# Kernel tuning notes

Hardware: AMD Instinct MI355X
Metric: run time of the kernel (lower is better)

## Reference

```python
import jax, jax.numpy as jnp
import numpy as np

N_NODES = 100000
N_EDGES = 300000
D_IN = 256
D_OUT = 256
NEG_SLOPE = 0.2


def setup_inputs() -> dict:
    key = jax.random.key(0)
    ks = jax.random.split(key, 6)
    feat = jax.random.normal(ks[0], (N_NODES, D_IN), dtype=jnp.float32)
    # xavier-normal-ish init scale
    scale = (2.0 / (D_IN + D_OUT)) ** 0.5
    W_src = jax.random.normal(ks[1], (D_IN, D_OUT), dtype=jnp.float32) * scale
    b_src = jnp.zeros((D_OUT,), dtype=jnp.float32)
    W_dst = jax.random.normal(ks[2], (D_IN, D_OUT), dtype=jnp.float32) * scale
    b_dst = jnp.zeros((D_OUT,), dtype=jnp.float32)
    attn = jax.random.normal(ks[3], (D_OUT,), dtype=jnp.float32) * scale
    src = jax.random.randint(ks[4], (N_EDGES,), 0, N_NODES, dtype=jnp.int32)
    dst = jax.random.randint(ks[5], (N_EDGES,), 0, N_NODES, dtype=jnp.int32)
    return {"feat": feat, "W_src": W_src, "b_src": b_src,
            "W_dst": W_dst, "b_dst": b_dst, "attn": attn,
            "src": src, "dst": dst}


def reference(feat, W_src, b_src, W_dst, b_dst, attn, src, dst):
    N = feat.shape[0]
    # node projections (dense GEMMs)
    el = feat @ W_src + b_src          # [N, D_OUT]  (feat_src / 'el')
    er = feat @ W_dst + b_dst          # [N, D_OUT]  (feat_dst / 'er')
    # edge-wise u_add_v + LeakyReLU, then attention dot
    e = jax.nn.leaky_relu(el[src] + er[dst], NEG_SLOPE)  # [E, D_OUT]
    score = e @ attn                    # [E]  ((e*attn).sum(-1))
    # edge softmax segmented by destination node
    smax = jax.ops.segment_max(score, dst, num_segments=N)   # [N]
    ex = jnp.exp(score - smax[dst])                           # [E]
    ssum = jax.ops.segment_sum(ex, dst, num_segments=N)      # [N]
    a = ex / ssum[dst]                                        # [E]
    # weighted scatter-sum aggregation: u_mul_e('el','a') -> sum per dst
    out = jax.ops.segment_sum(el[src] * a[:, None], dst, num_segments=N)
    return out  # [N, D_OUT]
```

## Files before the change

### kernel.cpp

```cpp
#include <hip/hip_runtime.h>
#include <cstdint>
#include <cmath>

#define D 256
#define NEG 0.2f
#define BK 64
#define NT (D/BK)

typedef __attribute__((ext_vector_type(8))) __bf16 bf16x8;
typedef __attribute__((ext_vector_type(8))) unsigned short ushort8;
typedef __attribute__((ext_vector_type(4))) float f32x4;

__device__ __forceinline__ unsigned short f2bf(float f){
    unsigned u = __float_as_uint(f);
    return (unsigned short)((u + 0x7fffu + ((u >> 16) & 1u)) >> 16);
}
__device__ __forceinline__ float b2f(unsigned short u){
    return __uint_as_float(((unsigned)u) << 16);
}

__device__ __forceinline__ void gload_lds16(const void* g, void* l){
    __builtin_amdgcn_global_load_lds(
        (const __attribute__((address_space(1))) unsigned int*)g,
        (__attribute__((address_space(3))) unsigned int*)l, 16, 0, 0);
}

__global__ __launch_bounds__(256) void prep_all_kernel(
    const float* __restrict__ Wsrc, const float* __restrict__ Wdst,
    const float* __restrict__ bsrc, const float* __restrict__ bdst,
    unsigned short* __restrict__ WT, float* __restrict__ biascat,
    const float* __restrict__ feat, unsigned short* __restrict__ featb,
    int N, int NPAD,
    const int* __restrict__ dst, int* __restrict__ deg, int E, int CB)
{
    const int b = blockIdx.x;
    if (b < 64) {
        int idx = b*256 + threadIdx.x;
        int col = idx >> 5;
        int u   = idx & 31;
        int gu  = (u & 24) | ((u ^ col) & 7);
        const float* W = (col < 256) ? Wsrc : Wdst;
        int c = col & 255;
        ushort8 o;
        #pragma unroll
        for (int j = 0; j < 8; ++j)
            o[j] = f2bf(W[(size_t)(gu*8 + j)*D + c]);
        *(ushort8*)(WT + (size_t)col*D + u*8) = o;
        if (idx < 512) biascat[idx] = (idx < 256) ? bsrc[idx] : bdst[idx-256];
    } else if (b < 64 + CB) {
        int e = (b - 64)*256 + threadIdx.x;
        if (e < E) atomicAdd(&deg[dst[e]], 1);
    } else {
        int nfb   = gridDim.x - 64 - CB;
        int total = NPAD * 32;
        for (int idx = (b - 64 - CB)*256 + threadIdx.x; idx < total; idx += nfb*256){
            int r = idx >> 5;
            int u = idx & 31;
            ushort8 o;
            if (r < N){
                int gu = (u & 24) | ((u ^ r) & 7);
                const float* s = feat + (size_t)r*D + gu*8;
                float4 a = *(const float4*)s;
                float4 bb = *(const float4*)(s + 4);
                o[0]=f2bf(a.x); o[1]=f2bf(a.y); o[2]=f2bf(a.z); o[3]=f2bf(a.w);
                o[4]=f2bf(bb.x); o[5]=f2bf(bb.y); o[6]=f2bf(bb.z); o[7]=f2bf(bb.w);
            } else {
                #pragma unroll
                for (int j = 0; j < 8; ++j) o[j] = 0;
            }
            *(ushort8*)(featb + (size_t)r*D + u*8) = o;
        }
    }
}

__global__ __launch_bounds__(256) void proj_mfma_kernel(
    const unsigned short* __restrict__ featb, const unsigned short* __restrict__ WT,
    const float* __restrict__ biascat,
    unsigned short* __restrict__ el16, unsigned short* __restrict__ er16, int N)
{
    __shared__ unsigned short As[2][128*BK];
    __shared__ unsigned short Bs[2][128*BK];

    const int b    = blockIdx.x;
    const int xcd  = b & 7;
    const int s    = b >> 3;
    const int p    = (s >> 2)*8 + xcd;
    const int c    = s & 3;
    const int row0 = p * 128;
    const int col0 = c * 128;

    const int tid  = threadIdx.x;
    const int wave = tid >> 6;
    const int lane = tid & 63;
    const int wr = (wave >> 1) * 64;
    const int wc = (wave & 1) * 64;
    const int l15 = lane & 15;
    const int kg  = lane >> 4;

    const int sr = (wave << 3) + (lane >> 3);
    const int sc = (lane & 7) * 8;

    f32x4 acc[4][4] = {};

    #pragma unroll
    for (int r4 = 0; r4 < 4; ++r4) {
        int ar = r4*32 + sr;
        gload_lds16(featb + (size_t)(row0 + ar)*D + 0 + sc, &As[0][(r4*32 + wave*8)*BK]);
        gload_lds16(WT    + (size_t)(col0 + ar)*D + 0 + sc, &Bs[0][(r4*32 + wave*8)*BK]);
    }

    for (int t = 0; t < NT; ++t) {
        const int cur = t & 1;
        if (t + 1 < NT) {
            int k0 = (t + 1) * BK;
            #pragma unroll
            for (int r4 = 0; r4 < 4; ++r4) {
                int ar = r4*32 + sr;
                gload_lds16(featb + (size_t)(row0 + ar)*D + k0 + sc,
                            &As[cur ^ 1][(r4*32 + wave*8)*BK]);
                gload_lds16(WT    + (size_t)(col0 + ar)*D + k0 + sc,
                            &Bs[cur ^ 1][(r4*32 + wave*8)*BK]);
            }
            asm volatile("s_waitcnt vmcnt(8)" ::: "memory");
        } else {
            asm volatile("s_waitcnt vmcnt(0)" ::: "memory");
        }
        __builtin_amdgcn_s_barrier();
        __builtin_amdgcn_sched_barrier(0);

        #pragma unroll
        for (int ks = 0; ks < 2; ++ks) {
            bf16x8 af[4], bfr[4];
            #pragma unroll
            for (int m = 0; m < 4; ++m){
                int row = wr + m*16 + l15;
                int cc = ((kg + ks*4) ^ (row & 7)) * 8;
                af[m] = *(const bf16x8*)&As[cur][row*BK + cc];
            }
            #pragma unroll
            for (int n = 0; n < 4; ++n){
                int row = wc + n*16 + l15;
                int cc = ((kg + ks*4) ^ (row & 7)) * 8;
                bfr[n] = *(const bf16x8*)&Bs[cur][row*BK + cc];
            }
            #pragma unroll
            for (int m = 0; m < 4; ++m)
                #pragma unroll
                for (int n = 0; n < 4; ++n)
                    acc[m][n] = __builtin_amdgcn_mfma_f32_16x16x32_bf16(bfr[n], af[m], acc[m][n], 0, 0, 0);
        }
        __builtin_amdgcn_sched_barrier(0);
        __builtin_amdgcn_s_barrier();
    }

    unsigned short* __restrict__ dstp = (col0 < 256) ? el16 : er16;
    const int ccbase = col0 & 255;
    #pragma unroll
    for (int m = 0; m < 4; ++m) {
        int row = row0 + wr + m*16 + l15;
        if (row >= N) continue;
        #pragma unroll
        for (int n = 0; n < 4; ++n) {
            int cw = wc + n*16 + kg*4;
            float4 b4 = *(const float4*)(biascat + col0 + cw);
            ushort4 o;
            o.x = f2bf(acc[m][n][0] + b4.x);
            o.y = f2bf(acc[m][n][1] + b4.y);
            o.z = f2bf(acc[m][n][2] + b4.z);
            o.w = f2bf(acc[m][n][3] + b4.w);
            *(ushort4*)(dstp + (size_t)row*D + ccbase + cw) = o;
        }
    }
}

__global__ __launch_bounds__(256) void scan1_kernel(const int* __restrict__ deg,
                                                    int* __restrict__ incl,
                                                    int* __restrict__ bsum, int N){
    __shared__ int s[256];
    int i = blockIdx.x*256 + threadIdx.x;
    int v = (i < N) ? deg[i] : 0;
    s[threadIdx.x] = v;
    __syncthreads();
    #pragma unroll
    for (int off = 1; off < 256; off <<= 1){
        int t = (threadIdx.x >= off) ? s[threadIdx.x - off] : 0;
        __syncthreads();
        s[threadIdx.x] += t;
        __syncthreads();
    }
    if (i < N) incl[i] = s[threadIdx.x];
    if (threadIdx.x == 255) bsum[blockIdx.x] = s[255];
}

__global__ __launch_bounds__(256) void scan23_kernel(const int* __restrict__ deg,
                                                     const int* __restrict__ incl,
                                                     const int* __restrict__ bsum,
                                                     int* __restrict__ rowstart,
                                                     int* __restrict__ cursor, int N){
    __shared__ int sbase;
    int b = blockIdx.x;
    if (threadIdx.x < 64){
        int acc = 0;
        for (int i = threadIdx.x; i < b; i += 64) acc += bsum[i];
        #pragma unroll
        for (int off = 32; off > 0; off >>= 1) acc += __shfl_xor(acc, off, 64);
        if (threadIdx.x == 0) sbase = acc;
    }
    __syncthreads();
    int i = b*256 + threadIdx.x;
    if (i < N){
        int st = incl[i] - deg[i] + sbase;
        rowstart[i] = st;
        cursor[i]   = st;
    }
}

__global__ void scatter_kernel(const int* __restrict__ dst, const int* __restrict__ src,
                               int* __restrict__ cursor, int* __restrict__ srcs, int E){
    int e = blockIdx.x*blockDim.x + threadIdx.x;
    if (e < E){
        int pos = atomicAdd(&cursor[dst[e]], 1);
        srcs[pos] = src[e];
    }
}

__global__ __launch_bounds__(256) void gat_node_kernel(
    const unsigned short* __restrict__ el16, const unsigned short* __restrict__ er16,
    const float* __restrict__ attn, const int* __restrict__ srcs,
    const int* __restrict__ rowstart, const int* __restrict__ degv,
    float* __restrict__ out, int N)
{
    int node = blockIdx.x*4 + (threadIdx.x >> 6);
    if (node >= N) return;
    int lane = threadIdx.x & 63;
    float4 o = make_float4(0.f,0.f,0.f,0.f);
    int deg = degv[node];
    float* op = out + (size_t)node*D + lane*4;
    if (deg == 0){ *(float4*)op = o; return; }

    ushort4 rv = *(const ushort4*)(er16 + (size_t)node*D + lane*4);
    float4 r4 = make_float4(b2f(rv.x), b2f(rv.y), b2f(rv.z), b2f(rv.w));
    float4 a4 = *(const float4*)(attn + lane*4);
    int start = rowstart[node];

    float m = -INFINITY, ssum = 0.f;
    for (int base = 0; base < deg; base += 4){
        int cnt = deg - base; if (cnt > 4) cnt = 4;
        float4 l[4]; float p[4];
        #pragma unroll
        for (int j = 0; j < 4; ++j){
            int k = base + j; if (k >= deg) k = deg - 1;
            int sn = srcs[start + k];
            ushort4 lv = *(const ushort4*)(el16 + (size_t)sn*D + lane*4);
            l[j] = make_float4(b2f(lv.x), b2f(lv.y), b2f(lv.z), b2f(lv.w));
        }
        #pragma unroll
        for (int j = 0; j < 4; ++j){
            float x, pp = 0.f;
            x = l[j].x + r4.x; pp += (x > 0.f ? x : NEG*x) * a4.x;
            x = l[j].y + r4.y; pp += (x > 0.f ? x : NEG*x) * a4.y;
            x = l[j].z + r4.z; pp += (x > 0.f ? x : NEG*x) * a4.z;
            x = l[j].w + r4.w; pp += (x > 0.f ? x : NEG*x) * a4.w;
            p[j] = pp;
        }
        #pragma unroll
        for (int off = 32; off > 0; off >>= 1){
            #pragma unroll
            for (int j = 0; j < 4; ++j) p[j] += __shfl_xor(p[j], off, 64);
        }
        #pragma unroll
        for (int j = 0; j < 4; ++j){
            if (j >= cnt) break;
            float newm  = fmaxf(m, p[j]);
            float scale = __expf(m - newm);
            float w     = __expf(p[j] - newm);
            ssum = ssum*scale + w;
            o.x = o.x*scale + w*l[j].x;
            o.y = o.y*scale + w*l[j].y;
            o.z = o.z*scale + w*l[j].z;
            o.w = o.w*scale + w*l[j].w;
            m = newm;
        }
    }
    float inv = 1.f/ssum;
    o.x *= inv; o.y *= inv; o.z *= inv; o.w *= inv;
    *(float4*)op = o;
}

extern "C" void kernel_launch(void* const* d_in, const int* in_sizes, int n_in,
                              void* d_out, int out_size, void* d_ws, size_t ws_size,
                              hipStream_t stream)
{
    const float* feat = (const float*)d_in[0];
    const float* Wsrc = (const float*)d_in[1];
    const float* bsrc = (const float*)d_in[2];
    const float* Wdst = (const float*)d_in[3];
    const float* bdst = (const float*)d_in[4];
    const float* attn = (const float*)d_in[5];
    const int*   src  = (const int*)d_in[6];
    const int*   dst  = (const int*)d_in[7];
    const int N = in_sizes[0] / D;
    const int E = in_sizes[6];
    const int NPAD = ((N + 1023)/1024)*1024;
    const int NP = NPAD / 128;
    float* out = (float*)d_out;

    unsigned short* el16 = (unsigned short*)d_ws;
    unsigned short* er16 = el16 + (size_t)N*D;
    int* deg      = (int*)(er16 + (size_t)N*D);
    int* incl     = deg + N;
    int* rowstart = incl + N;
    int* cursor   = rowstart + N;
    int* bsum     = cursor + N;
    int* srcs     = bsum + 512;
    unsigned short* WT = (unsigned short*)(srcs + E);
    float* biascat = (float*)(WT + (size_t)512*D);
    unsigned short* featb = (unsigned short*)(biascat + 512);

    const int nb = (N + 255)/256;
    const int CB = (E + 255)/256;

    hipMemsetAsync(deg, 0, (size_t)N*sizeof(int), stream);

    prep_all_kernel<<<64 + CB + 4096, 256, 0, stream>>>(
        Wsrc, Wdst, bsrc, bdst, WT, biascat, feat, featb, N, NPAD, dst, deg, E, CB);

    proj_mfma_kernel<<<4*NP, 256, 0, stream>>>(featb, WT, biascat, el16, er16, N);

    scan1_kernel<<<nb, 256, 0, stream>>>(deg, incl, bsum, N);
    scan23_kernel<<<nb, 256, 0, stream>>>(deg, incl, bsum, rowstart, cursor, N);
    scatter_kernel<<<(E + 255)/256, 256, 0, stream>>>(dst, src, cursor, srcs, E);

    gat_node_kernel<<<(N + 3)/4, 256, 0, stream>>>(el16, er16, attn, srcs,
                                                   rowstart, deg, out, N);
}
```

Before: 178.6 us.

## Give each wave private LDS tiles in projection GEMM, removing block barriers

The projection GEMM no longer shares 128-row A/B tiles across the block with double buffering. Each wave now loads its own 64x64 A and B sub-tiles into private LDS regions, so both s_barrier calls go away. In exchange, each wave loads its tiles redundantly, so global and L2 traffic per block doubles. Double buffering is also gone: every k-step waits for its loads to finish before the MFMAs run, so load latency is no longer hidden within a wave.

After: 184.6 us. 1.03x slower.

```diff
diff --git a/kernel.cpp b/kernel.cpp
--- a/kernel.cpp
+++ b/kernel.cpp
@@ -78,8 +78,8 @@
     const float* __restrict__ biascat,
     unsigned short* __restrict__ el16, unsigned short* __restrict__ er16, int N)
 {
-    __shared__ unsigned short As[2][128*BK];
-    __shared__ unsigned short Bs[2][128*BK];
+    __shared__ unsigned short As[4][64*BK];
+    __shared__ unsigned short Bs[4][64*BK];
 
     const int b    = blockIdx.x;
     const int xcd  = b & 7;
@@ -97,35 +97,24 @@
     const int l15 = lane & 15;
     const int kg  = lane >> 4;
 
-    const int sr = (wave << 3) + (lane >> 3);
-    const int sc = (lane & 7) * 8;
+    const int srow = lane >> 3;
+    const int suu  = lane & 7;
+
+    unsigned short* As_w = &As[wave][0];
+    unsigned short* Bs_w = &Bs[wave][0];
+    const unsigned short* Abase = featb + (size_t)(row0 + wr)*D;
+    const unsigned short* Bbase = WT    + (size_t)(col0 + wc)*D;
 
     f32x4 acc[4][4] = {};
 
-    #pragma unroll
-    for (int r4 = 0; r4 < 4; ++r4) {
-        int ar = r4*32 + sr;
-        gload_lds16(featb + (size_t)(row0 + ar)*D + 0 + sc, &As[0][(r4*32 + wave*8)*BK]);
-        gload_lds16(WT    + (size_t)(col0 + ar)*D + 0 + sc, &Bs[0][(r4*32 + wave*8)*BK]);
-    }
-
     for (int t = 0; t < NT; ++t) {
-        const int cur = t & 1;
-        if (t + 1 < NT) {
-            int k0 = (t + 1) * BK;
-            #pragma unroll
-            for (int r4 = 0; r4 < 4; ++r4) {
-                int ar = r4*32 + sr;
-                gload_lds16(featb + (size_t)(row0 + ar)*D + k0 + sc,
-                            &As[cur ^ 1][(r4*32 + wave*8)*BK]);
-                gload_lds16(WT    + (size_t)(col0 + ar)*D + k0 + sc,
-                            &Bs[cur ^ 1][(r4*32 + wave*8)*BK]);
-            }
-            asm volatile("s_waitcnt vmcnt(8)" ::: "memory");
-        } else {
-            asm volatile("s_waitcnt vmcnt(0)" ::: "memory");
-        }
-        __builtin_amdgcn_s_barrier();
+        const int k0 = t*BK;
+        #pragma unroll
+        for (int g = 0; g < 8; ++g) {
+            gload_lds16(Abase + (size_t)(g*8 + srow)*D + k0 + suu*8, As_w + g*512);
+            gload_lds16(Bbase + (size_t)(g*8 + srow)*D + k0 + suu*8, Bs_w + g*512);
+        }
+        asm volatile("s_waitcnt vmcnt(0)" ::: "memory");
         __builtin_amdgcn_sched_barrier(0);
 
         #pragma unroll
@@ -133,15 +122,15 @@
             bf16x8 af[4], bfr[4];
             #pragma unroll
             for (int m = 0; m < 4; ++m){
-                int row = wr + m*16 + l15;
-                int cc = ((kg + ks*4) ^ (row & 7)) * 8;
-                af[m] = *(const bf16x8*)&As[cur][row*BK + cc];
+                int lr = m*16 + l15;
+                int cc = ((kg + ks*4) ^ (lr & 7)) * 8;
+                af[m] = *(const bf16x8*)&As_w[lr*BK + cc];
             }
             #pragma unroll
             for (int n = 0; n < 4; ++n){
-                int row = wc + n*16 + l15;
-                int cc = ((kg + ks*4) ^ (row & 7)) * 8;
-                bfr[n] = *(const bf16x8*)&Bs[cur][row*BK + cc];
+                int lr = n*16 + l15;
+                int cc = ((kg + ks*4) ^ (lr & 7)) * 8;
+                bfr[n] = *(const bf16x8*)&Bs_w[lr*BK + cc];
             }
             #pragma unroll
             for (int m = 0; m < 4; ++m)
@@ -149,8 +138,8 @@
                 for (int n = 0; n < 4; ++n)
                     acc[m][n] = __builtin_amdgcn_mfma_f32_16x16x32_bf16(bfr[n], af[m], acc[m][n], 0, 0, 0);
         }
+        asm volatile("s_waitcnt lgkmcnt(0)" ::: "memory");
         __builtin_amdgcn_sched_barrier(0);
-        __builtin_amdgcn_s_barrier();
     }
 
     unsigned short* __restrict__ dstp = (col0 < 256) ? el16 : er16;
```
